# Kernel optimization log

Measured on AMD Instinct MI355X. Metric: run time of the kernel, lower is better.

## Reference

```python
import jax, jax.numpy as jnp
import numpy as np

B, S, DA, DV, DU, L, M = 16, 256, 1, 32, 1, 4, 12


def conv1x1(x, w, b):
    # x: [B,C,H,W], w: [O,C], b: [O]
    return jnp.einsum('bchw,oc->bohw', x, w) + b[None, :, None, None]


def setup_inputs() -> dict:
    key = jax.random.key(0)
    ks = jax.random.split(key, 12)
    sc = 0.02
    return {
        'x':    jax.random.normal(ks[0], (B, S, S, DA), dtype=jnp.float32),
        'p_w':  sc * jax.random.normal(ks[1], (DV, DA + 2), dtype=jnp.float32),
        'p_b':  sc * jax.random.normal(ks[2], (DV,), dtype=jnp.float32),
        'ws_w': sc * jax.random.normal(ks[3], (L, DV, DV), dtype=jnp.float32),
        'ws_b': sc * jax.random.normal(ks[4], (L, DV), dtype=jnp.float32),
        'w1r':  sc * jax.random.normal(ks[5], (L, DV, DV, M, M), dtype=jnp.float32),
        'w1i':  sc * jax.random.normal(ks[6], (L, DV, DV, M, M), dtype=jnp.float32),
        'w2r':  sc * jax.random.normal(ks[7], (L, DV, DV, M, M), dtype=jnp.float32),
        'w2i':  sc * jax.random.normal(ks[8], (L, DV, DV, M, M), dtype=jnp.float32),
        'q_w':  sc * jax.random.normal(ks[9], (DU, DV), dtype=jnp.float32),
        'q_b':  sc * jax.random.normal(ks[10], (DU,), dtype=jnp.float32),
    }


def fourier_layer(x, w1r, w1i, w2r, w2i):
    # x: [B,C,H,W]; FFT norm None == 'backward' (numpy/jax default)
    b, c, h, w = x.shape
    x_ft = jnp.fft.rfft2(x)                       # [B,C,H,W//2+1] complex
    W1 = w1r + 1j * w1i                           # [C,C,M,M]
    W2 = w2r + 1j * w2i
    top = jnp.einsum('bixy,ioxy->boxy', x_ft[:, :, :M, :M], W1)
    bot = jnp.einsum('bixy,ioxy->boxy', x_ft[:, :, -M:, :M], W2)
    out_ft = jnp.zeros((b, c, h, w // 2 + 1), dtype=x_ft.dtype)
    out_ft = out_ft.at[:, :, :M, :M].set(top)
    out_ft = out_ft.at[:, :, h - M:, :M].set(bot)
    return jnp.fft.irfft2(out_ft, s=(h, w))


def reference(x, p_w, p_b, ws_w, ws_b, w1r, w1i, w2r, w2i, q_w, q_b):
    b, sx, sy, _ = x.shape
    # grid as in get_grid (requires sx == sy, as the original implicitly does)
    gx = jnp.linspace(-1.0, 1.0, sx, dtype=jnp.float32)
    gy = jnp.linspace(-1.0, 1.0, sy, dtype=jnp.float32)
    gridx = jnp.broadcast_to(gx.reshape(1, 1, sx, 1), (b, sy, sx, 1))
    gridy = jnp.broadcast_to(gy.reshape(1, sy, 1, 1), (b, sy, sx, 1))
    grid = jnp.concatenate([gridy, gridx], axis=-1)     # [B,Sy,Sx,2]
    h = jnp.concatenate([x, grid], axis=-1)             # [B,S,S,DA+2]
    h = jnp.transpose(h, (0, 3, 1, 2))                  # NCHW
    h = conv1x1(h, p_w, p_b)                            # lifting
    for i in range(L):
        x1 = fourier_layer(h, w1r[i], w1i[i], w2r[i], w2i[i])
        x2 = conv1x1(h, ws_w[i], ws_b[i])
        h = x1 + x2
        if i < L - 1:
            h = jax.nn.relu(h)
    h = conv1x1(h, q_w, q_b)                            # projection -> [B,1,S,S]
    return jnp.transpose(h, (0, 2, 3, 1)).squeeze(-1)   # [B,S,S]
```

## Files before the change

### kernel.cpp

```cpp
#include <hip/hip_runtime.h>
#include <math.h>

#define NB 16
#define SS 256
#define DV 32
#define MM 12
#define MK 24
#define LL 4
#define TWO_PI_N 0.024543692606170259679f
#define HSTR 257
#define SEGOFF (DV * HSTR)

typedef float v2f __attribute__((ext_vector_type(2)));


__global__ __launch_bounds__(256) void k_prep(const float* __restrict__ ws_w,
        float* __restrict__ twT, float* __restrict__ wT, float* __restrict__ tw2)
{
    int j = threadIdx.x;
    #pragma unroll
    for (int k = 0; k < MM; ++k) {
        float ang = TWO_PI_N * (float)((k * j) & 255);
        float s, c; sincosf(ang, &s, &c);
        twT[j * (MM * 2) + 2 * k]     = c;
        twT[j * (MM * 2) + 2 * k + 1] = -s;
        tw2[(k * SS + j) * 2]     = c;
        tw2[(k * SS + j) * 2 + 1] = s;
    }
    for (int idx = threadIdx.x; idx < LL * DV * DV; idx += 256) {
        int l = idx >> 10, rem = idx & 1023, co = rem >> 5, ci = rem & 31;
        wT[(l * DV + ci) * DV + co] = ws_w[(l * DV + co) * DV + ci];
    }
}

__device__ __forceinline__ void row_dft_from_lds(float* smem,
        const float* __restrict__ twT, float* __restrict__ A,
        int b, int iy, int tid)
{
    int c   = tid & 31;
    int seg = tid >> 5;
    int j0  = seg << 5;

    v2f arai[MM];
    #pragma unroll
    for (int k = 0; k < MM; ++k) arai[k] = (v2f)(0.f);

    const float* hp = smem + c * HSTR + j0;
    #pragma unroll 2
    for (int i = 0; i < 32; ++i) {
        float v = hp[i];
        const v2f* twj = (const v2f*)(twT + (size_t)i * (MM * 2));
        #pragma unroll
        for (int k = 0; k < MM; ++k)
            arai[k] += twj[k] * v;
    }

    const float* ph = smem + SEGOFF + seg * (MM * 2);
    #pragma unroll
    for (int k = 0; k < MM; ++k) {
        float pr = ph[2 * k], pi = ph[2 * k + 1];
        float re = arai[k].x * pr - arai[k].y * pi;
        float im = arai[k].x * pi + arai[k].y * pr;
        arai[k].x = re; arai[k].y = im;
    }

    __syncthreads();
    v2f* red = (v2f*)smem;
    #pragma unroll
    for (int k = 0; k < MM; ++k) red[tid * 13 + k] = arai[k];
    __syncthreads();

    #pragma unroll
    for (int rep = 0; rep < 2; ++rep) {
        int o = tid + rep * 256;
        if (o < 384) {
            int k = o >> 5, cc = o & 31;
            v2f s = (v2f)(0.f);
            #pragma unroll
            for (int sg = 0; sg < 8; ++sg)
                s += red[(sg * 32 + cc) * 13 + k];
            size_t off = ((((size_t)(b * SS + iy)) * MM + k) * DV + cc) * 2;
            A[off]     = s.x;
            A[off + 1] = s.y;
        }
    }
}

__device__ __forceinline__ void build_segphase(float* smem, int tid)
{
    if (tid < 8 * MM) {
        int s = tid / MM, k = tid - s * MM;
        float ang = TWO_PI_N * (float)(((k * s) << 5) & 255);
        float sn, cs; sincosf(ang, &sn, &cs);
        smem[SEGOFF + 2 * tid]     = cs;
        smem[SEGOFF + 2 * tid + 1] = -sn;
    }
}

__global__ __launch_bounds__(256, 4) void k_liftdft(const float* __restrict__ x,
        const float* __restrict__ p_w, const float* __restrict__ p_b,
        float* __restrict__ h, const float* __restrict__ twT, float* __restrict__ A)
{
    __shared__ float smem[SEGOFF + 8 * MM * 2];
    int tid = threadIdx.x;
    int b  = blockIdx.x >> 8;
    int iy = blockIdx.x & 255;
    int j  = tid;

    build_segphase(smem, tid);

    float xv = x[((size_t)(b * SS + iy)) * SS + j];
    float gy = -1.f + 2.f * (float)iy * (1.f / 255.f);
    float gx = -1.f + 2.f * (float)j  * (1.f / 255.f);

    float* hb = h + ((size_t)b * DV * SS + iy) * SS + j;
    #pragma unroll
    for (int c = 0; c < DV; ++c) {
        float v = p_w[3*c] * xv + p_w[3*c+1] * gy + p_w[3*c+2] * gx + p_b[c];
        *(hb + (size_t)c * SS * SS) = v;
        smem[c * HSTR + j] = v;
    }
    __syncthreads();
    row_dft_from_lds(smem, twT, A, b, iy, tid);
}

__global__ __launch_bounds__(256, 2) void k_ptdft(float* __restrict__ h,
        const float* __restrict__ g, const float* __restrict__ wT,
        const float* __restrict__ ws_b, const float* __restrict__ tw2,
        const float* __restrict__ twT, float* __restrict__ A, int l)
{
    __shared__ float smem[SEGOFF + 8 * MM * 2];
    int tid = threadIdx.x;
    int b  = blockIdx.x >> 8;
    int iy = blockIdx.x & 255;
    int j  = tid;

    build_segphase(smem, tid);

    float* hb = h + ((size_t)b * DV * SS + iy) * SS + j;
    const float* wt  = wT + (size_t)l * DV * DV;
    const float* wsb = ws_b + (size_t)l * DV;

    float hv[DV];
    #pragma unroll
    for (int ci = 0; ci < DV; ++ci)
        hv[ci] = *(hb + (size_t)ci * SS * SS);

    float acc[DV];
    #pragma unroll
    for (int co = 0; co < DV; ++co) acc[co] = wsb[co];

    const float* gp = g + ((size_t)(b * SS + iy)) * (MM * DV * 2);
    #pragma unroll 2
    for (int ky = 0; ky < MM; ++ky) {
        float2 t2 = *(const float2*)(tw2 + ((size_t)ky * SS + j) * 2);
        const float* Gk = gp + ky * (DV * 2);
        #pragma unroll
        for (int co = 0; co < DV; ++co) {
            float gr = Gk[2 * co], gi = Gk[2 * co + 1];
            acc[co] += gr * t2.x - gi * t2.y;
        }
    }

    #pragma unroll 4
    for (int ci = 0; ci < DV; ++ci) {
        const float* wc = wt + ci * DV;
        #pragma unroll
        for (int co = 0; co < DV; ++co) acc[co] += wc[co] * hv[ci];
    }

    #pragma unroll
    for (int co = 0; co < DV; ++co) {
        float v = fmaxf(acc[co], 0.f);
        *(hb + (size_t)co * SS * SS) = v;
        smem[co * HSTR + j] = v;
    }
    __syncthreads();
    row_dft_from_lds(smem, twT, A, b, iy, tid);
}

__global__ __launch_bounds__(256, 4) void k_cm(const float* __restrict__ A,
        const float* __restrict__ w1r, const float* __restrict__ w1i,
        const float* __restrict__ w2r, const float* __restrict__ w2i,
        float* __restrict__ F, int l)
{
    __shared__ float red[4][DV][7][2];
    __shared__ float FinS[DV][6][2];
    int blk = blockIdx.x;
    int mg = blk & 3;
    int bk = blk >> 2;
    int b  = bk / MM;
    int ky = bk - b * MM;
    int tid = threadIdx.x;
    int c = tid & 31, ch = tid >> 5;
    int iy0 = ch * 32;

    const float2* Ap = (const float2*)(A) + ((size_t)(b * SS) * MM + ky) * DV + c;

    float fr[6], fi[6], pc[6], ps[6], sc[6], ssn[6];
    #pragma unroll
    for (int k = 0; k < 6; ++k) {
        int m = mg * 6 + k;
        int f = (m < MM) ? m : (232 + m);
        float s, cc;
        sincosf(TWO_PI_N * (float)f, &s, &cc);
        sc[k] = cc; ssn[k] = s;
        sincosf(TWO_PI_N * (float)((f * iy0) & 255), &s, &cc);
        pc[k] = cc; ps[k] = s;
        fr[k] = fi[k] = 0.f;
    }
    #pragma unroll 4
    for (int i = 0; i < 32; ++i) {
        float2 a = Ap[(size_t)(iy0 + i) * (MM * DV)];
        #pragma unroll
        for (int k = 0; k < 6; ++k) {
            fr[k] += a.x * pc[k] + a.y * ps[k];
            fi[k] += a.y * pc[k] - a.x * ps[k];
            float np = pc[k] * sc[k] - ps[k] * ssn[k];
            float nq = pc[k] * ssn[k] + ps[k] * sc[k];
            pc[k] = np; ps[k] = nq;
        }
    }
    #pragma unroll
    for (int k = 0; k < 6; ++k) {
        fr[k] += __shfl_xor(fr[k], 32, 64);
        fi[k] += __shfl_xor(fi[k], 32, 64);
    }
    int wv = tid >> 6;
    if ((tid & 63) < 32) {
        #pragma unroll
        for (int k = 0; k < 6; ++k) {
            red[wv][c][k][0] = fr[k];
            red[wv][c][k][1] = fi[k];
        }
    }
    __syncthreads();
    if (tid < 192) {
        int cc = tid & 31, k2 = tid >> 5;
        float sr = 0.f, si = 0.f;
        #pragma unroll
        for (int w = 0; w < 4; ++w) {
            sr += red[w][cc][k2][0];
            si += red[w][cc][k2][1];
        }
        FinS[cc][k2][0] = sr; FinS[cc][k2][1] = si;
    }
    __syncthreads();

    int c2 = tid >> 3, ch2 = tid & 7;
    if (ch2 < 6) {
        int o = c2;
        int m = mg * 6 + ch2;
        const float* Wr; const float* Wi; int xm;
        if (m < MM) { Wr = w1r; Wi = w1i; xm = m; }
        else        { Wr = w2r; Wi = w2i; xm = m - MM; }
        float scale = ((ky == 0) ? 1.0f : 2.0f) * (1.0f / 65536.0f);
        float orr = 0.f, oii = 0.f;
        #pragma unroll 4
        for (int i = 0; i < DV; ++i) {
            float gr = FinS[i][ch2][0], gi = FinS[i][ch2][1];
            size_t wi = ((size_t)(l * DV + i) * DV + o) * (MM * MM) + xm * MM + ky;
            float wr = Wr[wi], wim = Wi[wi];
            orr += gr * wr - gi * wim;
            oii += gr * wim + gi * wr;
        }
        size_t off = (((size_t)bk * MK + m) * DV + o) * 2;
        F[off] = orr * scale; F[off + 1] = oii * scale;
    }
}

__global__ __launch_bounds__(384) void k_inv1(const float* __restrict__ F,
        float* __restrict__ g)
{
    __shared__ float itw[MK * 2];
    int tid = threadIdx.x;
    int b = blockIdx.x >> 8, iy = blockIdx.x & 255;
    if (tid < MK) {
        int f = (tid < MM) ? tid : (232 + tid);
        float ang = TWO_PI_N * (float)((f * iy) & 255);
        float s, c; sincosf(ang, &s, &c);
        itw[2 * tid] = c; itw[2 * tid + 1] = s;
    }
    __syncthreads();

    int ky = tid >> 5, co = tid & 31;
    const float* Fp = F + ((size_t)(b * MM + ky) * MK) * (DV * 2) + 2 * co;
    float gr = 0.f, gi = 0.f;
    #pragma unroll
    for (int m = 0; m < MK; ++m) {
        float2 fv = *(const float2*)(Fp + (size_t)m * (DV * 2));
        float ic = itw[2 * m], is = itw[2 * m + 1];
        gr += fv.x * ic - fv.y * is;
        gi += fv.x * is + fv.y * ic;
    }
    size_t o = (((size_t)(b * SS + iy)) * MM + ky) * (DV * 2) + 2 * co;
    g[o] = gr; g[o + 1] = gi;
}

template<int FINAL>
__global__ __launch_bounds__(256, 4) void k_pt(float* __restrict__ h,
        const float* __restrict__ g, const float* __restrict__ wT,
        const float* __restrict__ ws_b, const float* __restrict__ tw2,
        const float* __restrict__ q_w, const float* __restrict__ q_b,
        float* __restrict__ out, int l)
{
    int tid = threadIdx.x;
    int lane = tid & 63;
    int w = __builtin_amdgcn_readfirstlane(tid >> 6);
    int b  = blockIdx.x >> 7;
    int iy = ((blockIdx.x & 127) << 1) + (w >> 1);
    int j0 = ((w & 1) << 7) + (lane << 1);

    float* hb = h + ((size_t)b * DV * SS + iy) * SS + j0;
    const float* wt  = wT + (size_t)l * DV * DV;
    const float* wsb = ws_b + (size_t)l * DV;

    float2 acc[DV];
    #pragma unroll
    for (int co = 0; co < DV; ++co) {
        float bv = wsb[co];
        acc[co].x = bv; acc[co].y = bv;
    }

    #pragma unroll 4
    for (int ci = 0; ci < DV; ++ci) {
        float2 hv = *(const float2*)(hb + (size_t)ci * SS * SS);
        const float* wc = wt + ci * DV;
        #pragma unroll
        for (int co = 0; co < DV; ++co) {
            float wv = wc[co];
            acc[co].x += wv * hv.x; acc[co].y += wv * hv.y;
        }
    }

    const float* gp = g + ((size_t)(b * SS + iy)) * (MM * DV * 2);
    #pragma unroll 2
    for (int ky = 0; ky < MM; ++ky) {
        float4 t4 = *(const float4*)(tw2 + ((size_t)ky * SS + j0) * 2);
        const float* Gk = gp + ky * (DV * 2);
        #pragma unroll
        for (int co = 0; co < DV; ++co) {
            float gr = Gk[2 * co], gi = Gk[2 * co + 1];
            acc[co].x += gr * t4.x - gi * t4.y;
            acc[co].y += gr * t4.z - gi * t4.w;
        }
    }

    if (FINAL) {
        float qb = q_b[0];
        float2 o2; o2.x = qb; o2.y = qb;
        #pragma unroll
        for (int co = 0; co < DV; ++co) {
            float qv = q_w[co];
            o2.x += qv * acc[co].x; o2.y += qv * acc[co].y;
        }
        *(float2*)(out + ((size_t)(b * SS + iy)) * SS + j0) = o2;
    } else {
        #pragma unroll
        for (int co = 0; co < DV; ++co) {
            float2 v;
            v.x = fmaxf(acc[co].x, 0.f); v.y = fmaxf(acc[co].y, 0.f);
            *(float2*)(hb + (size_t)co * SS * SS) = v;
        }
    }
}

extern "C" void kernel_launch(void* const* d_in, const int* in_sizes, int n_in,
                              void* d_out, int out_size, void* d_ws, size_t ws_size,
                              hipStream_t stream)
{
    const float* x    = (const float*)d_in[0];
    const float* p_w  = (const float*)d_in[1];
    const float* p_b  = (const float*)d_in[2];
    const float* ws_w = (const float*)d_in[3];
    const float* ws_b = (const float*)d_in[4];
    const float* w1r  = (const float*)d_in[5];
    const float* w1i  = (const float*)d_in[6];
    const float* w2r  = (const float*)d_in[7];
    const float* w2i  = (const float*)d_in[8];
    const float* q_w  = (const float*)d_in[9];
    const float* q_b  = (const float*)d_in[10];
    float* out = (float*)d_out;

    float* h   = (float*)d_ws;
    float* A   = h   + (size_t)NB * DV * SS * SS;
    float* F   = A   + (size_t)NB * SS * MM * DV * 2;
    float* g   = F   + (size_t)NB * MM * MK * DV * 2;
    float* twT = g   + (size_t)NB * SS * MM * DV * 2;
    float* wT  = twT + (size_t)SS * MM * 2;
    float* tw2 = wT  + (size_t)LL * DV * DV;

    dim3 blk(256);
    k_prep<<<1, blk, 0, stream>>>(ws_w, twT, wT, tw2);
    k_liftdft<<<NB * SS, blk, 0, stream>>>(x, p_w, p_b, h, twT, A);
    for (int l = 0; l < LL; ++l) {
        k_cm<<<NB * MM * 4, blk, 0, stream>>>(A, w1r, w1i, w2r, w2i, F, l);
        k_inv1<<<NB * SS, dim3(384), 0, stream>>>(F, g);
        if (l < LL - 1)
            k_ptdft<<<NB * SS, blk, 0, stream>>>(h, g, wT, ws_b, tw2, twT, A, l);
        else
            k_pt<1><<<NB * 128, blk, 0, stream>>>(h, g, wT, ws_b, tw2,
                                                  q_w, q_b, out, l);
    }
}
```

Before: 815.1 us.

## Exploit linearity of lifting to DFT only the scalar input row

```diff
diff --git a/kernel.cpp b/kernel.cpp
--- a/kernel.cpp
+++ b/kernel.cpp
@@ -15,7 +15,8 @@
 
 
 __global__ __launch_bounds__(256) void k_prep(const float* __restrict__ ws_w,
-        float* __restrict__ twT, float* __restrict__ wT, float* __restrict__ tw2)
+        float* __restrict__ twT, float* __restrict__ wT, float* __restrict__ tw2,
+        float* __restrict__ Gt)
 {
     int j = threadIdx.x;
     #pragma unroll
@@ -30,6 +31,17 @@
     for (int idx = threadIdx.x; idx < LL * DV * DV; idx += 256) {
         int l = idx >> 10, rem = idx & 1023, co = rem >> 5, ci = rem & 31;
         wT[(l * DV + ci) * DV + co] = ws_w[(l * DV + co) * DV + ci];
+    }
+    if (threadIdx.x < MM) {
+        int k = threadIdx.x;
+        float sr = 0.f, si = 0.f;
+        for (int jj = 0; jj < SS; ++jj) {
+            float gxv = -1.f + 2.f * (float)jj * (1.f / 255.f);
+            float s, c; sincosf(TWO_PI_N * (float)((k * jj) & 255), &s, &c);
+            sr += gxv * c;
+            si -= gxv * s;
+        }
+        Gt[2 * k] = sr; Gt[2 * k + 1] = si;
     }
 }
 
@@ -97,9 +109,93 @@
     }
 }
 
-__global__ __launch_bounds__(256, 4) void k_liftdft(const float* __restrict__ x,
+__global__ __launch_bounds__(256, 4) void k_lift(const float* __restrict__ x,
         const float* __restrict__ p_w, const float* __restrict__ p_b,
-        float* __restrict__ h, const float* __restrict__ twT, float* __restrict__ A)
+        float* __restrict__ h, const float* __restrict__ twT,
+        const float* __restrict__ Gt, float* __restrict__ A)
+{
+    __shared__ float sx[SS];
+    __shared__ float sX[MM * 2];
+    int tid = threadIdx.x;
+    int b  = blockIdx.x >> 8;
+    int iy = blockIdx.x & 255;
+    int j  = tid;
+
+    float xv = x[((size_t)(b * SS + iy)) * SS + j];
+    sx[j] = xv;
+    float gy = -1.f + 2.f * (float)iy * (1.f / 255.f);
+    float gx = -1.f + 2.f * (float)j  * (1.f / 255.f);
+
+    float* hb = h + ((size_t)b * DV * SS + iy) * SS + j;
+    #pragma unroll
+    for (int c = 0; c < DV; ++c) {
+        float v = p_w[3*c] * xv + p_w[3*c+1] * gy + p_w[3*c+2] * gx + p_b[c];
+        *(hb + (size_t)c * SS * SS) = v;
+    }
+    __syncthreads();
+
+    if (tid < 64) {
+        int s = tid >> 3, q = tid & 7;
+        v2f ar[MM];
+        #pragma unroll
+        for (int k = 0; k < MM; ++k) ar[k] = (v2f)(0.f);
+        #pragma unroll
+        for (int ii = 0; ii < 4; ++ii) {
+            int jj = (s << 5) + q + (ii << 3);
+            float v = sx[jj];
+            const v2f* twj = (const v2f*)(twT + (size_t)jj * (MM * 2));
+            #pragma unroll
+            for (int k = 0; k < MM; ++k)
+                ar[k] += twj[k] * v;
+        }
+        #pragma unroll
+        for (int k = 0; k < MM; ++k) {
+            float sn, cs; sincosf(TWO_PI_N * (float)(((k * s) << 5) & 255), &sn, &cs);
+            float pr = cs, pi = -sn;
+            float re = ar[k].x * pr - ar[k].y * pi;
+            float im = ar[k].x * pi + ar[k].y * pr;
+            ar[k].x = re; ar[k].y = im;
+        }
+        #pragma unroll
+        for (int m = 1; m < 64; m <<= 1) {
+            #pragma unroll
+            for (int k = 0; k < MM; ++k) {
+                ar[k].x += __shfl_xor(ar[k].x, m, 64);
+                ar[k].y += __shfl_xor(ar[k].y, m, 64);
+            }
+        }
+        if (tid == 0) {
+            #pragma unroll
+            for (int k = 0; k < MM; ++k) {
+                sX[2 * k]     = ar[k].x;
+                sX[2 * k + 1] = ar[k].y;
+            }
+        }
+    }
+    __syncthreads();
+
+    #pragma unroll
+    for (int rep = 0; rep < 2; ++rep) {
+        int o = tid + rep * 256;
+        if (o < MM * DV) {
+            int k = o >> 5, cc = o & 31;
+            float Xr = sX[2 * k], Xi = sX[2 * k + 1];
+            float Gr = Gt[2 * k], Gi = Gt[2 * k + 1];
+            float w0 = p_w[3 * cc], w2 = p_w[3 * cc + 2];
+            float ar2 = w0 * Xr + w2 * Gr;
+            float ai2 = w0 * Xi + w2 * Gi;
+            if (k == 0) ar2 += 256.f * (p_w[3 * cc + 1] * gy + p_b[cc]);
+            size_t off = ((((size_t)(b * SS + iy)) * MM + k) * DV + cc) * 2;
+            A[off]     = ar2;
+            A[off + 1] = ai2;
+        }
+    }
+}
+
+__global__ __launch_bounds__(256, 4) void k_ptdft(float* __restrict__ h,
+        const float* __restrict__ g, const float* __restrict__ wT,
+        const float* __restrict__ ws_b, const float* __restrict__ tw2,
+        const float* __restrict__ twT, float* __restrict__ A, int l)
 {
     __shared__ float smem[SEGOFF + 8 * MM * 2];
     int tid = threadIdx.x;
@@ -109,71 +205,45 @@
 
     build_segphase(smem, tid);
 
-    float xv = x[((size_t)(b * SS + iy)) * SS + j];
-    float gy = -1.f + 2.f * (float)iy * (1.f / 255.f);
-    float gx = -1.f + 2.f * (float)j  * (1.f / 255.f);
-
-    float* hb = h + ((size_t)b * DV * SS + iy) * SS + j;
-    #pragma unroll
-    for (int c = 0; c < DV; ++c) {
-        float v = p_w[3*c] * xv + p_w[3*c+1] * gy + p_w[3*c+2] * gx + p_b[c];
-        *(hb + (size_t)c * SS * SS) = v;
-        smem[c * HSTR + j] = v;
-    }
-    __syncthreads();
-    row_dft_from_lds(smem, twT, A, b, iy, tid);
-}
-
-__global__ __launch_bounds__(256, 2) void k_ptdft(float* __restrict__ h,
-        const float* __restrict__ g, const float* __restrict__ wT,
-        const float* __restrict__ ws_b, const float* __restrict__ tw2,
-        const float* __restrict__ twT, float* __restrict__ A, int l)
-{
-    __shared__ float smem[SEGOFF + 8 * MM * 2];
-    int tid = threadIdx.x;
-    int b  = blockIdx.x >> 8;
-    int iy = blockIdx.x & 255;
-    int j  = tid;
-
-    build_segphase(smem, tid);
-
     float* hb = h + ((size_t)b * DV * SS + iy) * SS + j;
     const float* wt  = wT + (size_t)l * DV * DV;
     const float* wsb = ws_b + (size_t)l * DV;
 
-    float hv[DV];
-    #pragma unroll
-    for (int ci = 0; ci < DV; ++ci)
-        hv[ci] = *(hb + (size_t)ci * SS * SS);
-
-    float acc[DV];
-    #pragma unroll
-    for (int co = 0; co < DV; ++co) acc[co] = wsb[co];
+    v2f acc2[16];
+    #pragma unroll
+    for (int p = 0; p < 16; ++p) acc2[p] = *(const v2f*)(wsb + 2 * p);
+
+    #pragma unroll 4
+    for (int ci = 0; ci < DV; ++ci) {
+        float hv = *(hb + (size_t)ci * SS * SS);
+        const v2f* wcp = (const v2f*)(wt + ci * DV);
+        #pragma unroll
+        for (int p = 0; p < 16; ++p) acc2[p] += wcp[p] * hv;
+    }
 
     const float* gp = g + ((size_t)(b * SS + iy)) * (MM * DV * 2);
     #pragma unroll 2
     for (int ky = 0; ky < MM; ++ky) {
         float2 t2 = *(const float2*)(tw2 + ((size_t)ky * SS + j) * 2);
         const float* Gk = gp + ky * (DV * 2);
-        #pragma unroll
-        for (int co = 0; co < DV; ++co) {
-            float gr = Gk[2 * co], gi = Gk[2 * co + 1];
-            acc[co] += gr * t2.x - gi * t2.y;
-        }
-    }
-
-    #pragma unroll 4
-    for (int ci = 0; ci < DV; ++ci) {
-        const float* wc = wt + ci * DV;
-        #pragma unroll
-        for (int co = 0; co < DV; ++co) acc[co] += wc[co] * hv[ci];
-    }
-
-    #pragma unroll
-    for (int co = 0; co < DV; ++co) {
-        float v = fmaxf(acc[co], 0.f);
-        *(hb + (size_t)co * SS * SS) = v;
-        smem[co * HSTR + j] = v;
+        const v2f* grp = (const v2f*)(Gk);
+        const v2f* gip = (const v2f*)(Gk + DV);
+        float nt2y = -t2.y;
+        #pragma unroll
+        for (int p = 0; p < 16; ++p) {
+            acc2[p] += grp[p] * t2.x;
+            acc2[p] += gip[p] * nt2y;
+        }
+    }
+
+    #pragma unroll
+    for (int p = 0; p < 16; ++p) {
+        float v0 = fmaxf(acc2[p].x, 0.f);
+        float v1 = fmaxf(acc2[p].y, 0.f);
+        *(hb + (size_t)(2 * p)     * SS * SS) = v0;
+        *(hb + (size_t)(2 * p + 1) * SS * SS) = v1;
+        smem[(2 * p)     * HSTR + j] = v0;
+        smem[(2 * p + 1) * HSTR + j] = v1;
     }
     __syncthreads();
     row_dft_from_lds(smem, twT, A, b, iy, tid);
@@ -293,8 +363,9 @@
         gr += fv.x * ic - fv.y * is;
         gi += fv.x * is + fv.y * ic;
     }
-    size_t o = (((size_t)(b * SS + iy)) * MM + ky) * (DV * 2) + 2 * co;
-    g[o] = gr; g[o + 1] = gi;
+    size_t o = (((size_t)(b * SS + iy)) * MM + ky) * (DV * 2);
+    g[o + co]      = gr;
+    g[o + DV + co] = gi;
 }
 
 template<int FINAL>
@@ -340,7 +411,7 @@
         const float* Gk = gp + ky * (DV * 2);
         #pragma unroll
         for (int co = 0; co < DV; ++co) {
-            float gr = Gk[2 * co], gi = Gk[2 * co + 1];
+            float gr = Gk[co], gi = Gk[DV + co];
             acc[co].x += gr * t4.x - gi * t4.y;
             acc[co].y += gr * t4.z - gi * t4.w;
         }
@@ -389,10 +460,11 @@
     float* twT = g   + (size_t)NB * SS * MM * DV * 2;
     float* wT  = twT + (size_t)SS * MM * 2;
     float* tw2 = wT  + (size_t)LL * DV * DV;
+    float* Gt  = tw2 + (size_t)MM * SS * 2;
 
     dim3 blk(256);
-    k_prep<<<1, blk, 0, stream>>>(ws_w, twT, wT, tw2);
-    k_liftdft<<<NB * SS, blk, 0, stream>>>(x, p_w, p_b, h, twT, A);
+    k_prep<<<1, blk, 0, stream>>>(ws_w, twT, wT, tw2, Gt);
+    k_lift<<<NB * SS, blk, 0, stream>>>(x, p_w, p_b, h, twT, Gt, A);
     for (int l = 0; l < LL; ++l) {
         k_cm<<<NB * MM * 4, blk, 0, stream>>>(A, w1r, w1i, w2r, w2i, F, l);
         k_inv1<<<NB * SS, dim3(384), 0, stream>>>(F, g);
```

Measured after the change: 690.2 us. 15.3% less time.
